# Optimization experiments

Measured on AMD Instinct MI355X. Metric: run time of the kernel, lower is better.

Reference implementation:

```python
import jax, jax.numpy as jnp
import numpy as np

E = 8      # num routed experts
H = 1024   # hidden_size
I = 1408   # moe_intermediate_size
T = 2048   # tokens (batch*seq flattened)
K = 2      # top_k experts per token


def setup_inputs() -> dict:
    key = jax.random.key(0)
    k1, k2, k3, k4, k5 = jax.random.split(key, 5)
    x = jax.random.normal(k1, (T, H), dtype=jnp.float32)
    expert_ids = jax.random.randint(k2, (T, K), 0, E, dtype=jnp.int64)
    routing_weights = jax.random.uniform(k3, (T, K), dtype=jnp.float32)
    # kaiming_uniform_(a=sqrt(5)) on 2D tensor -> bound = 1/sqrt(fan_in), fan_in = dim1
    b1 = 1.0 / np.sqrt(2 * I)
    w1 = jax.random.uniform(k4, (E * H, 2 * I), dtype=jnp.float32, minval=-b1, maxval=b1)
    b2 = 1.0 / np.sqrt(H)
    w2 = jax.random.uniform(k5, (E * I, H), dtype=jnp.float32, minval=-b2, maxval=b2)
    return {"x": x, "expert_ids": expert_ids, "routing_weights": routing_weights,
            "w1": w1, "w2": w2}


def reference(x, expert_ids, routing_weights, w1, w2):
    # Fused routed MLP: per token, for each of its top-k experts e with gate p:
    #   out += p * (silu(x @ W1_gate[e]) * (x @ W1_up[e])) @ W2[e]
    w1r = w1.reshape(E, H, 2 * I)   # fused gate+up per expert
    w2r = w2.reshape(E, I, H)       # down proj per expert

    h = jnp.einsum('th,ehi->eti', x, w1r)           # [E, T, 2I]
    gate, up = h[..., :I], h[..., I:]
    act = jax.nn.silu(gate) * up                    # [E, T, I]
    y = jnp.einsum('eti,eih->eth', act, w2r)        # [E, T, H]

    # combine weights: [T, E] = sum over the k slots of onehot(expert)*routing_weight
    disp = jnp.sum(jax.nn.one_hot(expert_ids, E, dtype=x.dtype)
                   * routing_weights[..., None], axis=1)  # [T, E]
    out = jnp.einsum('eth,te->th', y, disp)         # [T, H]
    return out
```

## Files before the change

kernel.cpp:

```cpp
#include <hip/hip_runtime.h>
#include <hip/hip_bf16.h>
#include <math.h>

#define E    8
#define H    1024
#define I2   2816
#define II   1408
#define T    2048
#define KTOP 2
#define NP   (T * KTOP)

#define BM   128
#define BK   32
#define BNA  64
#define BN2  128
#define GX   40

#define CVT_BLKS   1024
#define TW1_PER_E  (44 * 16)
#define TW1_BLKS   (TW1_PER_E * E)
#define TW2_PER_E  (16 * 22)
#define TW2_BLKS   (TW2_PER_E * E)
#define PREP_BLKS  (CVT_BLKS + TW1_BLKS + TW2_BLKS + 1)

typedef __attribute__((ext_vector_type(8))) short  short8v;
typedef __attribute__((ext_vector_type(4))) float  f32x4;
typedef __attribute__((ext_vector_type(8))) unsigned short ushort8;

__device__ __forceinline__ void gload16(void* lds, const void* g) {
    __builtin_amdgcn_global_load_lds((const __attribute__((address_space(1))) unsigned int*)g,
                                     (__attribute__((address_space(3))) unsigned int*)lds,
                                     16, 0, 0);
}

union PrepShared {
    float tile[64][65];
    struct { int cnt[E]; int base[E + 1]; int pos[E]; } rt;
};

__device__ __forceinline__ void transpose_tile(const float* __restrict__ src,
                                               __hip_bfloat16* __restrict__ dst,
                                               int e, int n0, int k0, int K, int N,
                                               PrepShared& sh, int tid)
{
    const float* s = src + (size_t)e * K * N + (size_t)k0 * N + n0;
    int kr = tid >> 2;
    int nc = (tid & 3) * 16;
    const float* srow = s + (size_t)kr * N + nc;
#pragma unroll
    for (int i = 0; i < 4; ++i) {
        float4 v = *(const float4*)(srow + i * 4);
        sh.tile[kr][nc + i * 4 + 0] = v.x;
        sh.tile[kr][nc + i * 4 + 1] = v.y;
        sh.tile[kr][nc + i * 4 + 2] = v.z;
        sh.tile[kr][nc + i * 4 + 3] = v.w;
    }
    __syncthreads();
    int nr = tid >> 2;
    int kc = (tid & 3) * 16;
    alignas(16) __hip_bfloat16 tmp[16];
#pragma unroll
    for (int i = 0; i < 16; ++i) tmp[i] = __float2bfloat16(sh.tile[kc + i][nr]);
    __hip_bfloat16* drow = dst + (size_t)e * K * N + (size_t)(n0 + nr) * K + k0 + kc;
    *(ushort8*)(drow)     = *(ushort8*)tmp;
    *(ushort8*)(drow + 8) = *(ushort8*)(tmp + 8);
}

__launch_bounds__(256)
__global__ void prep_kernel(const float* __restrict__ x, const float* __restrict__ w1,
                            const float* __restrict__ w2, const int* __restrict__ ids,
                            __hip_bfloat16* __restrict__ xb,
                            __hip_bfloat16* __restrict__ w1t,
                            __hip_bfloat16* __restrict__ w2t,
                            int* __restrict__ tok, int* __restrict__ inv,
                            int* __restrict__ seg_off, int* __restrict__ tile_off)
{
    __shared__ PrepShared sh;
    int tid = threadIdx.x;
    int b = blockIdx.x;

    if (b < CVT_BLKS) {
        int i = (b * 256 + tid) * 8;
        float4 a = *(const float4*)(x + i);
        float4 c = *(const float4*)(x + i + 4);
        alignas(16) __hip_bfloat16 t[8];
        t[0] = __float2bfloat16(a.x); t[1] = __float2bfloat16(a.y);
        t[2] = __float2bfloat16(a.z); t[3] = __float2bfloat16(a.w);
        t[4] = __float2bfloat16(c.x); t[5] = __float2bfloat16(c.y);
        t[6] = __float2bfloat16(c.z); t[7] = __float2bfloat16(c.w);
        *(ushort8*)(xb + i) = *(ushort8*)t;
        return;
    }
    b -= CVT_BLKS;
    if (b < TW1_BLKS) {
        int e = b / TW1_PER_E, r = b % TW1_PER_E;
        transpose_tile(w1, w1t, e, (r % 44) * 64, (r / 44) * 64, H, I2, sh, tid);
        return;
    }
    b -= TW1_BLKS;
    if (b < TW2_BLKS) {
        int e = b / TW2_PER_E, r = b % TW2_PER_E;
        transpose_tile(w2, w2t, e, (r % 16) * 64, (r / 16) * 64, II, H, sh, tid);
        return;
    }

    if (tid < E) { sh.rt.cnt[tid] = 0; sh.rt.pos[tid] = 0; }
    __syncthreads();
    for (int p = tid; p < NP; p += 256) atomicAdd(&sh.rt.cnt[ids[p]], 1);
    __syncthreads();
    if (tid == 0) {
        int s = 0;
        for (int e = 0; e < E; ++e) { sh.rt.base[e] = s; s += sh.rt.cnt[e]; }
        sh.rt.base[E] = s;
    }
    __syncthreads();
    for (int p = tid; p < NP; p += 256) {
        int e = ids[p];
        int q = sh.rt.base[e] + atomicAdd(&sh.rt.pos[e], 1);
        tok[q] = p >> 1;
        inv[p] = q;
    }
    if (tid == 0) {
        int s = 0;
        for (int e = 0; e < E; ++e) {
            seg_off[e]  = sh.rt.base[e];
            tile_off[e] = s;
            s += (sh.rt.cnt[e] + BM - 1) / BM;
        }
        seg_off[E]  = sh.rt.base[E];
        tile_off[E] = s;
    }
}

__launch_bounds__(256, 2)
__global__ void gemm1_silu(const __hip_bfloat16* __restrict__ xb,
                           const __hip_bfloat16* __restrict__ w1t,
                           const int* __restrict__ tok,
                           const int* __restrict__ seg_off,
                           const int* __restrict__ tile_off,
                           __hip_bfloat16* __restrict__ act)
{
    __shared__ __align__(16) __hip_bfloat16 As[BM * BK];
    __shared__ __align__(16) __hip_bfloat16 Bg[BNA * BK];
    __shared__ __align__(16) __hip_bfloat16 Bu[BNA * BK];
    __shared__ int tokS[BM];

    int bx = blockIdx.x;
    if (bx >= tile_off[E]) return;
    int e = 0;
#pragma unroll
    for (int i = 1; i < E; ++i) if (bx >= tile_off[i]) e = i;
    int row0 = seg_off[e] + (bx - tile_off[e]) * BM;
    int rend = seg_off[e + 1];
    int jb   = blockIdx.y * BNA;

    int tid = threadIdx.x;
    if (tid < BM) {
        int gr = row0 + tid;
        tokS[tid] = tok[gr < NP ? gr : NP - 1];
    }
    __syncthreads();

    int arow = tid >> 2;
    int aoff = (tid & 3) * 16;
    const char* xB  = (const char*)xb;
    const char* w1B = (const char*)(w1t + (size_t)e * I2 * H);
    const char* srcA0 = xB + (size_t)tokS[arow]      * 2048 + aoff;
    const char* srcA1 = xB + (size_t)tokS[arow + 64] * 2048 + aoff;
    const char* srcG  = w1B + (size_t)(jb + arow)      * 2048 + aoff;
    const char* srcU  = w1B + (size_t)(II + jb + arow) * 2048 + aoff;
    __hip_bfloat16* dA0 = &As[tid * 8];
    __hip_bfloat16* dA1 = &As[2048 + tid * 8];
    __hip_bfloat16* dG  = &Bg[tid * 8];
    __hip_bfloat16* dU  = &Bu[tid * 8];

    int lane = tid & 63;
    int w  = tid >> 6;
    int wm = w >> 1, wn = w & 1;
    int fr = lane & 15;
    int kc = lane >> 4;

    f32x4 accg[4][2] = {};
    f32x4 accu[4][2] = {};
    const short8v* Asv = (const short8v*)As;
    const short8v* Bgv = (const short8v*)Bg;
    const short8v* Buv = (const short8v*)Bu;

    for (int k0 = 0; k0 < H; k0 += BK) {
        gload16(dA0, srcA0);
        gload16(dA1, srcA1);
        gload16(dG, srcG);
        gload16(dU, srcU);
        srcA0 += 64; srcA1 += 64; srcG += 64; srcU += 64;
        __syncthreads();

        short8v a[4], g[2], u[2];
#pragma unroll
        for (int m = 0; m < 4; ++m)
            a[m] = Asv[(wm * 64 + m * 16 + fr) * 4 + kc];
#pragma unroll
        for (int n = 0; n < 2; ++n) {
            g[n] = Bgv[(wn * 32 + n * 16 + fr) * 4 + kc];
            u[n] = Buv[(wn * 32 + n * 16 + fr) * 4 + kc];
        }
#pragma unroll
        for (int m = 0; m < 4; ++m)
#pragma unroll
            for (int n = 0; n < 2; ++n) {
                accg[m][n] = __builtin_amdgcn_mfma_f32_16x16x32_bf16(a[m], g[n], accg[m][n], 0, 0, 0);
                accu[m][n] = __builtin_amdgcn_mfma_f32_16x16x32_bf16(a[m], u[n], accu[m][n], 0, 0, 0);
            }
        __syncthreads();
    }

#pragma unroll
    for (int m = 0; m < 4; ++m)
#pragma unroll
        for (int n = 0; n < 2; ++n) {
            int col = jb + wn * 32 + n * 16 + fr;
#pragma unroll
            for (int j = 0; j < 4; ++j) {
                int gr = row0 + wm * 64 + m * 16 + kc * 4 + j;
                if (gr < rend) {
                    float gg = accg[m][n][j];
                    float s  = gg / (1.0f + __expf(-gg));
                    act[(size_t)gr * II + col] = __float2bfloat16(s * accu[m][n][j]);
                }
            }
        }
}

__launch_bounds__(256, 2)
__global__ void gemm2(const __hip_bfloat16* __restrict__ act,
                      const __hip_bfloat16* __restrict__ w2t,
                      const int* __restrict__ seg_off,
                      const int* __restrict__ tile_off,
                      float* __restrict__ y)
{
    __shared__ __align__(16) __hip_bfloat16 As[BM * BK];
    __shared__ __align__(16) __hip_bfloat16 Bs[BN2 * BK];

    int bx = blockIdx.x;
    if (bx >= tile_off[E]) return;
    int e = 0;
#pragma unroll
    for (int i = 1; i < E; ++i) if (bx >= tile_off[i]) e = i;
    int row0 = seg_off[e] + (bx - tile_off[e]) * BM;
    int rend = seg_off[e + 1];
    int nb   = blockIdx.y * BN2;

    int tid = threadIdx.x;
    int arow = tid >> 2;
    int aoff = (tid & 3) * 16;
    const char* actB = (const char*)act;
    const char* w2B  = (const char*)(w2t + (size_t)e * H * II);
    int r0c = row0 + arow;       r0c = r0c < NP ? r0c : NP - 1;
    int r1c = row0 + arow + 64;  r1c = r1c < NP ? r1c : NP - 1;
    const char* srcA0 = actB + (size_t)r0c * 2816 + aoff;
    const char* srcA1 = actB + (size_t)r1c * 2816 + aoff;
    const char* srcB0 = w2B + (size_t)(nb + arow)      * 2816 + aoff;
    const char* srcB1 = w2B + (size_t)(nb + arow + 64) * 2816 + aoff;
    __hip_bfloat16* dA0 = &As[tid * 8];
    __hip_bfloat16* dA1 = &As[2048 + tid * 8];
    __hip_bfloat16* dB0 = &Bs[tid * 8];
    __hip_bfloat16* dB1 = &Bs[2048 + tid * 8];

    int lane = tid & 63;
    int w  = tid >> 6;
    int wm = w >> 1, wn = w & 1;
    int fr = lane & 15;
    int kc = lane >> 4;

    f32x4 acc[4][4] = {};
    const short8v* Asv = (const short8v*)As;
    const short8v* Bsv = (const short8v*)Bs;

    for (int k0 = 0; k0 < II; k0 += BK) {
        gload16(dA0, srcA0);
        gload16(dA1, srcA1);
        gload16(dB0, srcB0);
        gload16(dB1, srcB1);
        srcA0 += 64; srcA1 += 64; srcB0 += 64; srcB1 += 64;
        __syncthreads();

        short8v a[4], b[4];
#pragma unroll
        for (int m = 0; m < 4; ++m)
            a[m] = Asv[(wm * 64 + m * 16 + fr) * 4 + kc];
#pragma unroll
        for (int n = 0; n < 4; ++n)
            b[n] = Bsv[(wn * 64 + n * 16 + fr) * 4 + kc];
#pragma unroll
        for (int m = 0; m < 4; ++m)
#pragma unroll
            for (int n = 0; n < 4; ++n)
                acc[m][n] = __builtin_amdgcn_mfma_f32_16x16x32_bf16(a[m], b[n], acc[m][n], 0, 0, 0);
        __syncthreads();
    }

#pragma unroll
    for (int m = 0; m < 4; ++m)
#pragma unroll
        for (int n = 0; n < 4; ++n) {
            int col = nb + wn * 64 + n * 16 + fr;
#pragma unroll
            for (int j = 0; j < 4; ++j) {
                int lr = wm * 64 + m * 16 + kc * 4 + j;
                int gr = row0 + lr;
                if (gr < rend)
                    y[(size_t)gr * H + col] = acc[m][n][j];
            }
        }
}

__global__ void gather_out(const float* __restrict__ y, const int* __restrict__ inv,
                           const float* __restrict__ rw, float* __restrict__ out)
{
    int gid = blockIdx.x * 256 + threadIdx.x;
    int t = gid >> 8;
    int c = (gid & 255) * 4;
    int q0 = inv[2 * t], q1 = inv[2 * t + 1];
    float w0 = rw[2 * t], w1 = rw[2 * t + 1];
    float4 a = *(const float4*)(y + (size_t)q0 * H + c);
    float4 b = *(const float4*)(y + (size_t)q1 * H + c);
    float4 o;
    o.x = w0 * a.x + w1 * b.x;
    o.y = w0 * a.y + w1 * b.y;
    o.z = w0 * a.z + w1 * b.z;
    o.w = w0 * a.w + w1 * b.w;
    *(float4*)(out + (size_t)t * H + c) = o;
}

extern "C" void kernel_launch(void* const* d_in, const int* in_sizes, int n_in,
                              void* d_out, int out_size, void* d_ws, size_t ws_size,
                              hipStream_t stream)
{
    const float* x   = (const float*)d_in[0];
    const int*   ids = (const int*)d_in[1];
    const float* rw  = (const float*)d_in[2];
    const float* w1  = (const float*)d_in[3];
    const float* w2  = (const float*)d_in[4];
    float*       out = (float*)d_out;

    char* ws = (char*)d_ws;
    int*   tok  = (int*)ws;
    int*   inv  = (int*)(ws + 16384);
    int*   seg  = (int*)(ws + 32768);
    int*   tile = (int*)(ws + 32768 + 64);
    __hip_bfloat16* xb  = (__hip_bfloat16*)(ws + 65536);
    __hip_bfloat16* w1t = (__hip_bfloat16*)(ws + 4259840);
    __hip_bfloat16* w2t = (__hip_bfloat16*)(ws + 50397184);
    __hip_bfloat16* act = (__hip_bfloat16*)(ws + 73465856);
    float*          y   = (float*)(ws + 85000192);

    prep_kernel<<<PREP_BLKS, 256, 0, stream>>>(x, w1, w2, ids, xb, w1t, w2t,
                                               tok, inv, seg, tile);

    gemm1_silu<<<dim3(GX, II / BNA), 256, 0, stream>>>(xb, w1t, tok, seg, tile, act);
    gemm2<<<dim3(GX, H / BN2), 256, 0, stream>>>(act, w2t, seg, tile, y);
    gather_out<<<(T * H) / (256 * 4), 256, 0, stream>>>(y, inv, rw, out);
}
```

Before: 278.0 us.

## Restructure prep kernel: strip transposes with swizzled bf16 LDS and ballot-based routing

```diff
diff --git a/kernel.cpp b/kernel.cpp
--- a/kernel.cpp
+++ b/kernel.cpp
@@ -16,12 +16,12 @@
 #define BN2  128
 #define GX   40
 
-#define CVT_BLKS   1024
-#define TW1_PER_E  (44 * 16)
-#define TW1_BLKS   (TW1_PER_E * E)
-#define TW2_PER_E  (16 * 22)
-#define TW2_BLKS   (TW2_PER_E * E)
-#define PREP_BLKS  (CVT_BLKS + TW1_BLKS + TW2_BLKS + 1)
+#define CVT_BLKS  1024
+#define W1_PER_E  (4 * 44)
+#define W1_BLKS   (W1_PER_E * E)
+#define W2_PER_E  (11 * 16)
+#define W2_BLKS   (W2_PER_E * E)
+#define PREP_BLKS (1 + CVT_BLKS + W1_BLKS + W2_BLKS)
 
 typedef __attribute__((ext_vector_type(8))) short  short8v;
 typedef __attribute__((ext_vector_type(4))) float  f32x4;
@@ -34,36 +34,83 @@
 }
 
 union PrepShared {
-    float tile[64][65];
-    struct { int cnt[E]; int base[E + 1]; int pos[E]; } rt;
+    char tiles[2][8192];
+    struct { int cnt4[4][E]; int woff[4][E]; } rt;
 };
 
-__device__ __forceinline__ void transpose_tile(const float* __restrict__ src,
-                                               __hip_bfloat16* __restrict__ dst,
-                                               int e, int n0, int k0, int K, int N,
-                                               PrepShared& sh, int tid)
-{
-    const float* s = src + (size_t)e * K * N + (size_t)k0 * N + n0;
-    int kr = tid >> 2;
-    int nc = (tid & 3) * 16;
-    const float* srow = s + (size_t)kr * N + nc;
+__device__ __forceinline__ void tr_load(const float* __restrict__ src, int K, int N,
+                                        int e, int n0, int krow0, int tid, float4* f)
+{
+    const float* s = src + (size_t)e * K * N + (size_t)(krow0 + (tid >> 2)) * N
+                     + n0 + (tid & 3) * 16;
+    f[0] = *(const float4*)(s);
+    f[1] = *(const float4*)(s + 4);
+    f[2] = *(const float4*)(s + 8);
+    f[3] = *(const float4*)(s + 12);
+}
+
+__device__ __forceinline__ void tr_write(char* lds, int tid, const float4* f)
+{
+    alignas(16) __hip_bfloat16 t[16];
 #pragma unroll
     for (int i = 0; i < 4; ++i) {
-        float4 v = *(const float4*)(srow + i * 4);
-        sh.tile[kr][nc + i * 4 + 0] = v.x;
-        sh.tile[kr][nc + i * 4 + 1] = v.y;
-        sh.tile[kr][nc + i * 4 + 2] = v.z;
-        sh.tile[kr][nc + i * 4 + 3] = v.w;
-    }
+        t[4 * i + 0] = __float2bfloat16(f[i].x);
+        t[4 * i + 1] = __float2bfloat16(f[i].y);
+        t[4 * i + 2] = __float2bfloat16(f[i].z);
+        t[4 * i + 3] = __float2bfloat16(f[i].w);
+    }
+    int r  = tid >> 2;
+    int cb = (tid & 3) * 32;
+    int sw = (r & 7) << 4;
+    *(ushort8*)(lds + r * 128 + ((cb)      ^ sw)) = ((ushort8*)t)[0];
+    *(ushort8*)(lds + r * 128 + ((cb + 16) ^ sw)) = ((ushort8*)t)[1];
+}
+
+__device__ __forceinline__ void tr_store(const char* lds0, const char* lds1,
+                                         __hip_bfloat16* __restrict__ dst, int K, int N,
+                                         int e, int n0, int kdst0, int tid)
+{
+    int g  = tid >> 7;
+    int h  = tid & 127;
+    int n  = h >> 1;
+    int kb = 32 * (h & 1);
+    const char* lds = g ? lds1 : lds0;
+    alignas(16) __hip_bfloat16 t[32];
+#pragma unroll
+    for (int j = 0; j < 32; ++j) {
+        int r = kb + j;
+        t[j] = *(const __hip_bfloat16*)(lds + r * 128 + ((2 * n) ^ ((r & 7) << 4)));
+    }
+    __hip_bfloat16* d = dst + (size_t)e * K * N + (size_t)(n0 + n) * K + kdst0 + 64 * g + kb;
+    *(ushort8*)(d)      = ((ushort8*)t)[0];
+    *(ushort8*)(d + 8)  = ((ushort8*)t)[1];
+    *(ushort8*)(d + 16) = ((ushort8*)t)[2];
+    *(ushort8*)(d + 24) = ((ushort8*)t)[3];
+}
+
+__device__ __forceinline__ void tr_strip(const float* __restrict__ src,
+                                         __hip_bfloat16* __restrict__ dst,
+                                         int K, int N, int e, int n0, int k0,
+                                         int np, PrepShared& sh, int tid)
+{
+    float4 fa0[4], fb0[4], fa1[4], fb1[4];
+    tr_load(src, K, N, e, n0, k0,      tid, fa0);
+    tr_load(src, K, N, e, n0, k0 + 64, tid, fb0);
+    if (np == 2) {
+        tr_load(src, K, N, e, n0, k0 + 128, tid, fa1);
+        tr_load(src, K, N, e, n0, k0 + 192, tid, fb1);
+    }
+    tr_write(sh.tiles[0], tid, fa0);
+    tr_write(sh.tiles[1], tid, fb0);
     __syncthreads();
-    int nr = tid >> 2;
-    int kc = (tid & 3) * 16;
-    alignas(16) __hip_bfloat16 tmp[16];
-#pragma unroll
-    for (int i = 0; i < 16; ++i) tmp[i] = __float2bfloat16(sh.tile[kc + i][nr]);
-    __hip_bfloat16* drow = dst + (size_t)e * K * N + (size_t)(n0 + nr) * K + k0 + kc;
-    *(ushort8*)(drow)     = *(ushort8*)tmp;
-    *(ushort8*)(drow + 8) = *(ushort8*)(tmp + 8);
+    tr_store(sh.tiles[0], sh.tiles[1], dst, K, N, e, n0, k0, tid);
+    if (np == 2) {
+        __syncthreads();
+        tr_write(sh.tiles[0], tid, fa1);
+        tr_write(sh.tiles[1], tid, fb1);
+        __syncthreads();
+        tr_store(sh.tiles[0], sh.tiles[1], dst, K, N, e, n0, k0 + 128, tid);
+    }
 }
 
 __launch_bounds__(256)
@@ -78,6 +125,65 @@
     __shared__ PrepShared sh;
     int tid = threadIdx.x;
     int b = blockIdx.x;
+
+    if (b == 0) {
+        int lane = tid & 63;
+        int w    = tid >> 6;
+        unsigned long long ltm = (1ull << lane) - 1ull;
+
+        int wc = 0;
+#pragma unroll 1
+        for (int it = 0; it < 16; ++it) {
+            int p = it * 256 + w * 64 + lane;
+            int e = ids[p];
+#pragma unroll
+            for (int ee = 0; ee < E; ++ee) {
+                unsigned long long m = __ballot(e == ee);
+                if (lane == ee) wc += (int)__popcll(m);
+            }
+        }
+        if (lane < E) sh.rt.cnt4[w][lane] = wc;
+        __syncthreads();
+        if (tid == 0) {
+            int base = 0, tiles = 0;
+            for (int e = 0; e < E; ++e) {
+                seg_off[e]  = base;
+                tile_off[e] = tiles;
+                int tot = 0;
+                for (int ww = 0; ww < 4; ++ww) {
+                    sh.rt.woff[ww][e] = base + tot;
+                    tot += sh.rt.cnt4[ww][e];
+                }
+                base  += tot;
+                tiles += (tot + BM - 1) / BM;
+            }
+            seg_off[E]  = base;
+            tile_off[E] = tiles;
+        }
+        __syncthreads();
+        int run = (lane < E) ? sh.rt.woff[w][lane] : 0;
+#pragma unroll 1
+        for (int it = 0; it < 16; ++it) {
+            int p = it * 256 + w * 64 + lane;
+            int e = ids[p];
+            unsigned long long me = 0;
+            int acnt = 0;
+#pragma unroll
+            for (int ee = 0; ee < E; ++ee) {
+                unsigned long long m = __ballot(e == ee);
+                if (e == ee) me = m;
+                if (lane == ee) acnt = (int)__popcll(m);
+            }
+            int rank = (int)__popcll(me & ltm);
+            int qb   = __shfl(run, e, 64);
+            int q    = qb + rank;
+            tok[q] = p >> 1;
+            inv[p] = q;
+            run += acnt;
+        }
+        return;
+    }
+    b -= 1;
 
     if (b < CVT_BLKS) {
         int i = (b * 256 + tid) * 8;
@@ -92,43 +198,16 @@
         return;
     }
     b -= CVT_BLKS;
-    if (b < TW1_BLKS) {
-        int e = b / TW1_PER_E, r = b % TW1_PER_E;
-        transpose_tile(w1, w1t, e, (r % 44) * 64, (r / 44) * 64, H, I2, sh, tid);
+
+    if (b < W1_BLKS) {
+        int e = b / W1_PER_E, r = b % W1_PER_E;
+        tr_strip(w1, w1t, H, I2, e, (r % 44) * 64, (r / 44) * 256, 2, sh, tid);
         return;
     }
-    b -= TW1_BLKS;
-    if (b < TW2_BLKS) {
-        int e = b / TW2_PER_E, r = b % TW2_PER_E;
-        transpose_tile(w2, w2t, e, (r % 16) * 64, (r / 16) * 64, II, H, sh, tid);
-        return;
-    }
-
-    if (tid < E) { sh.rt.cnt[tid] = 0; sh.rt.pos[tid] = 0; }
-    __syncthreads();
-    for (int p = tid; p < NP; p += 256) atomicAdd(&sh.rt.cnt[ids[p]], 1);
-    __syncthreads();
-    if (tid == 0) {
-        int s = 0;
-        for (int e = 0; e < E; ++e) { sh.rt.base[e] = s; s += sh.rt.cnt[e]; }
-        sh.rt.base[E] = s;
-    }
-    __syncthreads();
-    for (int p = tid; p < NP; p += 256) {
-        int e = ids[p];
-        int q = sh.rt.base[e] + atomicAdd(&sh.rt.pos[e], 1);
-        tok[q] = p >> 1;
-        inv[p] = q;
-    }
-    if (tid == 0) {
-        int s = 0;
-        for (int e = 0; e < E; ++e) {
-            seg_off[e]  = sh.rt.base[e];
-            tile_off[e] = s;
-            s += (sh.rt.cnt[e] + BM - 1) / BM;
-        }
-        seg_off[E]  = sh.rt.base[E];
-        tile_off[E] = s;
+    b -= W1_BLKS;
+    {
+        int e = b / W2_PER_E, r = b % W2_PER_E;
+        tr_strip(w2, w2t, II, H, e, (r % 16) * 64, (r / 16) * 128, 1, sh, tid);
     }
 }
 
```

Result: slower. 286.1 us (+2.9%).
